# Kernel tuning notes

Measured on AMD Instinct MI355X. Metric: run time of the kernel, lower is better.

## Reference

```python
import jax, jax.numpy as jnp
import numpy as np

WS = 4        # window size
NH = 8        # num heads
GN_GROUPS = 8 # min(8, hidden_dim)
EPS = 1e-5


def group_norm(x, gamma, beta, groups=GN_GROUPS, eps=EPS):
    # x: [B, C, H, W]
    B, C, H, W = x.shape
    xr = x.reshape(B, groups, C // groups, H, W)
    mu = xr.mean(axis=(2, 3, 4), keepdims=True)
    var = xr.var(axis=(2, 3, 4), keepdims=True)
    xn = ((xr - mu) / jnp.sqrt(var + eps)).reshape(B, C, H, W)
    return xn * gamma[None, :, None, None] + beta[None, :, None, None]


def setup_inputs() -> dict:
    key = jax.random.key(0)
    ks = jax.random.split(key, 8)
    B, Cin, Ch, H, W = 4, 64, 256, 128, 128
    sc = 0.02
    return {
        "x": jax.random.normal(ks[0], (B, Cin, H, W), dtype=jnp.float32),
        "h": jax.random.normal(ks[1], (B, Ch, H, W), dtype=jnp.float32),
        "c": jax.random.normal(ks[2], (B, Ch, H, W), dtype=jnp.float32),
        "in_proj_w": jax.random.normal(ks[3], (Ch, Cin + Ch), dtype=jnp.float32) * sc,
        "in_proj_b": jnp.zeros((Ch,), jnp.float32),
        "ln_g": jnp.ones((Ch,), jnp.float32),
        "ln_b": jnp.zeros((Ch,), jnp.float32),
        "qkv_w": jax.random.normal(ks[4], (3 * Ch, Ch), dtype=jnp.float32) * sc,
        "qkv_b": jnp.zeros((3 * Ch,), jnp.float32),
        "proj_w": jax.random.normal(ks[5], (Ch, Ch), dtype=jnp.float32) * sc,
        "proj_b": jnp.zeros((Ch,), jnp.float32),
        "gates_w": jax.random.normal(ks[6], (4 * Ch, Ch), dtype=jnp.float32) * sc,
        "gates_b": jnp.zeros((4 * Ch,), jnp.float32),
        "gn_g": jnp.ones((Ch,), jnp.float32),
        "gn_b": jnp.zeros((Ch,), jnp.float32),
    }


def reference(x, h, c, in_proj_w, in_proj_b, ln_g, ln_b, qkv_w, qkv_b,
              proj_w, proj_b, gates_w, gates_b, gn_g, gn_b):
    B, Cin, H, W = x.shape
    Ch = h.shape[1]
    ws, nh = WS, NH
    hd = Ch // nh
    nHw, nWw = H // ws, W // ws  # H,W divisible by ws -> no padding branch

    # in_proj: 1x1 conv on concat([x, h])
    comb = jnp.concatenate([x, h], axis=1)  # [B, Cin+Ch, H, W]
    p = jnp.einsum('bchw,oc->bohw', comb, in_proj_w) + in_proj_b[None, :, None, None]

    # window partition -> [B*nWin, ws*ws, Ch]
    xw = p.reshape(B, Ch, nHw, ws, nWw, ws)
    xw = xw.transpose(0, 2, 4, 3, 5, 1).reshape(B * nHw * nWw, ws * ws, Ch)

    # pre-attention LayerNorm
    mu = xw.mean(-1, keepdims=True)
    var = xw.var(-1, keepdims=True)
    xn = (xw - mu) / jnp.sqrt(var + EPS) * ln_g + ln_b

    # multi-head attention within each 16-token window
    Bw, N, _ = xn.shape
    qkv = (xn @ qkv_w.T + qkv_b).reshape(Bw, N, 3, nh, hd)
    q, k, v = qkv[:, :, 0], qkv[:, :, 1], qkv[:, :, 2]  # [Bw, N, nh, hd]
    attn = jnp.einsum('bqhd,bkhd->bhqk', q, k) * (hd ** -0.5)
    attn = jax.nn.softmax(attn, axis=-1)
    out = jnp.einsum('bhqk,bkhd->bqhd', attn, v).reshape(Bw, N, Ch)
    out = out @ proj_w.T + proj_b

    # window unpartition -> [B, Ch, H, W]
    am = out.reshape(B, nHw, nWw, ws, ws, Ch)
    am = am.transpose(0, 5, 1, 3, 2, 4).reshape(B, Ch, H, W)

    am = group_norm(am, gn_g, gn_b)  # eval mode: dropout2d is identity

    # LSTM gates via 1x1 conv
    gates = jnp.einsum('bchw,oc->bohw', am, gates_w) + gates_b[None, :, None, None]
    ci, cf, co, cg = jnp.split(gates, 4, axis=1)
    i = jax.nn.sigmoid(ci)
    f = jax.nn.sigmoid(cf)
    o = jax.nn.sigmoid(co)
    g = jnp.tanh(cg)
    cnext = f * c + i * g
    hnext = group_norm(o * jnp.tanh(cnext), gn_g, gn_b)
    return hnext, cnext
```

## Files before the change

kernel.cpp:

```cpp
#include <hip/hip_runtime.h>

#define DI __device__ __forceinline__

typedef unsigned short ushort_t;
typedef __attribute__((ext_vector_type(8))) short bf16x8;
typedef __attribute__((ext_vector_type(4))) float f32x4;
typedef __attribute__((ext_vector_type(4))) unsigned short us4;
typedef __attribute__((ext_vector_type(8))) unsigned short us8;

constexpr float EPSF = 1e-5f;

constexpr size_t O_WIP  = 0;
constexpr size_t O_WQKV = 163840;
constexpr size_t O_WPRJ = 557056;
constexpr size_t O_WGAT = 688128;
constexpr size_t O_GN   = 1736704;
constexpr size_t O_FIN  = 1737216;
constexpr size_t O_R2   = 1740800;
constexpr size_t O_R3   = O_R2 + 33554432;
constexpr size_t O_R1   = O_R3 + 33554432;

DI ushort_t f2b(float f) {
  unsigned u = __float_as_uint(f);
  u += 0x7fff + ((u >> 16) & 1);
  return (ushort_t)(u >> 16);
}
DI float b2f(ushort_t s) { return __uint_as_float(((unsigned)s) << 16); }

DI float fsig(float x) { return 1.f / (1.f + __expf(-x)); }
DI float ftanh(float x) {
  const float e = __expf(-2.f * fabsf(x));
  const float t = (1.f - e) / (1.f + e);
  return copysignf(t, x);
}

DI void cp16(ushort_t* lds, const ushort_t* g) {
  __builtin_amdgcn_global_load_lds(
      (const __attribute__((address_space(1))) unsigned*)g,
      (__attribute__((address_space(3))) unsigned*)lds, 16, 0, 0);
}

__global__ __launch_bounds__(256) void k_prep(const float* __restrict__ ipw,
    const float* __restrict__ qkvw, const float* __restrict__ projw,
    const float* __restrict__ gatesw, ushort_t* __restrict__ d0,
    ushort_t* __restrict__ d1, ushort_t* __restrict__ d2, ushort_t* __restrict__ d3) {
  int i = blockIdx.x * 256 + threadIdx.x;
  if (i < 81920)  { d0[i] = f2b(ipw[i]);    return; }
  i -= 81920;
  if (i < 196608) { d1[i] = f2b(qkvw[i]);   return; }
  i -= 196608;
  if (i < 65536)  { d2[i] = f2b(projw[i]);  return; }
  i -= 65536;
  if (i < 262144) { d3[i] = f2b(gatesw[i]); return; }
}

__global__ __launch_bounds__(256) void k_comb(const float* __restrict__ x,
    const float* __restrict__ h, ushort_t* __restrict__ comb) {
  __shared__ float tile[32][257];
  const int tid = threadIdx.x;
  const int wid = blockIdx.x;
  const int b = wid / 640, r = wid % 640, ct = r / 64, pt = r % 64;
  const int p0 = pt * 256;
#pragma unroll 8
  for (int i = 0; i < 32; ++i) {
    const int cg = ct * 32 + i;
    const float* src = (cg < 64) ? x + (((size_t)(b * 64 + cg)) << 14)
                                 : h + (((size_t)(b * 256 + (cg - 64))) << 14);
    tile[i][tid] = src[p0 + tid];
  }
  __syncthreads();
  const int c = tid & 31;
#pragma unroll 8
  for (int i2 = 0; i2 < 32; ++i2) {
    const int tl = (tid >> 5) + i2 * 8;
    comb[(size_t)((b << 14) + p0 + tl) * 320 + ct * 32 + c] = f2b(tile[c][tl]);
  }
}

template<int K, int KT, bool GATESB>
DI void gemm_main(const ushort_t* __restrict__ A, const ushort_t* __restrict__ B,
                  int t0, int nb, ushort_t* smem, f32x4 acc[4][4]) {
  const int tid = threadIdx.x;
  const int lane = tid & 63, wave = tid >> 6;
  const int w2 = wave * 2;
  const int wm = wave >> 1, wn = wave & 1;
  const int kfs = lane >> 4, cc = lane & 15;
  const int aoff = kfs * 1024 + (wm * 64 + cc) * 8;
  const int boff = 4096 + kfs * 1024 + (wn * 64 + cc) * 8;

  auto stage = [&](int buf, int k0) {
#pragma unroll
    for (int i = 0; i < 2; ++i) {
      const int w2i = w2 + i;
      const int kslot = w2i >> 1;
      const int mrow = ((w2i & 1) << 6) + lane;
      const ushort_t* ga = A + (size_t)(t0 + mrow) * K + k0 + kslot * 8;
      cp16(smem + buf * 8192 + w2i * 512, ga);
      int ng;
      if (GATESB) ng = ((mrow >> 4) & 3) * 256 + nb + ((mrow >> 6) << 4) + (mrow & 15);
      else        ng = nb + mrow;
      const ushort_t* gb = B + (size_t)ng * K + k0 + kslot * 8;
      cp16(smem + buf * 8192 + 4096 + w2i * 512, gb);
    }
  };

  stage(0, 0);
  __syncthreads();
  for (int kt = 0; kt < KT; ++kt) {
    const int cur = (kt & 1) * 8192;
    if (kt + 1 < KT) stage((kt & 1) ^ 1, (kt + 1) * 32);
    bf16x8 a0 = *(const bf16x8*)(smem + cur + aoff);
    bf16x8 a1 = *(const bf16x8*)(smem + cur + aoff + 128);
    bf16x8 a2 = *(const bf16x8*)(smem + cur + aoff + 256);
    bf16x8 a3 = *(const bf16x8*)(smem + cur + aoff + 384);
    bf16x8 b0 = *(const bf16x8*)(smem + cur + boff);
    bf16x8 b1 = *(const bf16x8*)(smem + cur + boff + 128);
    bf16x8 b2 = *(const bf16x8*)(smem + cur + boff + 256);
    bf16x8 b3 = *(const bf16x8*)(smem + cur + boff + 384);
    acc[0][0] = __builtin_amdgcn_mfma_f32_16x16x32_bf16(a0, b0, acc[0][0], 0, 0, 0);
    acc[0][1] = __builtin_amdgcn_mfma_f32_16x16x32_bf16(a0, b1, acc[0][1], 0, 0, 0);
    acc[0][2] = __builtin_amdgcn_mfma_f32_16x16x32_bf16(a0, b2, acc[0][2], 0, 0, 0);
    acc[0][3] = __builtin_amdgcn_mfma_f32_16x16x32_bf16(a0, b3, acc[0][3], 0, 0, 0);
    acc[1][0] = __builtin_amdgcn_mfma_f32_16x16x32_bf16(a1, b0, acc[1][0], 0, 0, 0);
    acc[1][1] = __builtin_amdgcn_mfma_f32_16x16x32_bf16(a1, b1, acc[1][1], 0, 0, 0);
    acc[1][2] = __builtin_amdgcn_mfma_f32_16x16x32_bf16(a1, b2, acc[1][2], 0, 0, 0);
    acc[1][3] = __builtin_amdgcn_mfma_f32_16x16x32_bf16(a1, b3, acc[1][3], 0, 0, 0);
    acc[2][0] = __builtin_amdgcn_mfma_f32_16x16x32_bf16(a2, b0, acc[2][0], 0, 0, 0);
    acc[2][1] = __builtin_amdgcn_mfma_f32_16x16x32_bf16(a2, b1, acc[2][1], 0, 0, 0);
    acc[2][2] = __builtin_amdgcn_mfma_f32_16x16x32_bf16(a2, b2, acc[2][2], 0, 0, 0);
    acc[2][3] = __builtin_amdgcn_mfma_f32_16x16x32_bf16(a2, b3, acc[2][3], 0, 0, 0);
    acc[3][0] = __builtin_amdgcn_mfma_f32_16x16x32_bf16(a3, b0, acc[3][0], 0, 0, 0);
    acc[3][1] = __builtin_amdgcn_mfma_f32_16x16x32_bf16(a3, b1, acc[3][1], 0, 0, 0);
    acc[3][2] = __builtin_amdgcn_mfma_f32_16x16x32_bf16(a3, b2, acc[3][2], 0, 0, 0);
    acc[3][3] = __builtin_amdgcn_mfma_f32_16x16x32_bf16(a3, b3, acc[3][3], 0, 0, 0);
    __syncthreads();
  }
}

template<int NTOT>
DI void epi_store(f32x4 acc[4][4], ushort_t* __restrict__ C, const float* __restrict__ bias,
                  int t0, int n0g) {
  const int tid = threadIdx.x, lane = tid & 63, wave = tid >> 6;
  const int wm = wave >> 1, wn = wave & 1;
  const int r0 = (lane >> 4) * 4, cc = lane & 15;
#pragma unroll
  for (int fn = 0; fn < 4; ++fn) {
    const int n = wn * 64 + fn * 16 + cc;
    const float bv = bias[n0g + n];
#pragma unroll
    for (int fm = 0; fm < 4; ++fm) {
#pragma unroll
      for (int r = 0; r < 4; ++r) {
        const int m = wm * 64 + fm * 16 + r0 + r;
        C[(size_t)(t0 + m) * NTOT + n0g + n] = f2b(acc[fm][fn][r] + bv);
      }
    }
  }
}

__global__ __launch_bounds__(256) void k_inproj_ln(const ushort_t* __restrict__ A,
    const ushort_t* __restrict__ B, const float* __restrict__ bias,
    const float* __restrict__ lg, const float* __restrict__ lb, ushort_t* __restrict__ xn) {
  __shared__ ushort_t smem[20480];
  __shared__ float red[4][2][64];
  __shared__ float fin[2][64];
  const int tid = threadIdx.x, lane = tid & 63, wave = tid >> 6;
  const int t0 = blockIdx.x * 64;
  const int kfs = lane >> 4, cc = lane & 15;
  const int r0 = kfs * 4;
  const int aoff = kfs * 512 + cc * 8;
  const int boff = 2048 + kfs * 2048 + (wave * 64 + cc) * 8;

  auto stage = [&](int buf, int k0) {
#pragma unroll
    for (int rr = 0; rr < 5; ++rr) {
      const int r = wave * 5 + rr;
      const int e = r * 64 + lane;
      const ushort_t* src;
      if (r < 4) src = A + (size_t)(t0 + (e & 63)) * 320 + k0 + (e >> 6) * 8;
      else { const int e2 = e - 256; src = B + (size_t)(e2 & 255) * 320 + k0 + (e2 >> 8) * 8; }
      cp16(smem + buf * 10240 + r * 512, src);
    }
  };

  stage(0, 0);
  f32x4 acc[4][4] = {};
  __syncthreads();
  for (int kt = 0; kt < 10; ++kt) {
    const int cur = (kt & 1) * 10240;
    if (kt < 9) stage((kt & 1) ^ 1, (kt + 1) * 32);
    bf16x8 av[4], bv[4];
#pragma unroll
    for (int i = 0; i < 4; ++i) av[i] = *(const bf16x8*)(smem + cur + aoff + i * 128);
#pragma unroll
    for (int j = 0; j < 4; ++j) bv[j] = *(const bf16x8*)(smem + cur + boff + j * 128);
#pragma unroll
    for (int i = 0; i < 4; ++i)
#pragma unroll
      for (int j = 0; j < 4; ++j)
        acc[i][j] = __builtin_amdgcn_mfma_f32_16x16x32_bf16(av[i], bv[j], acc[i][j], 0, 0, 0);
    __syncthreads();
  }
  float bcol[4];
#pragma unroll
  for (int j = 0; j < 4; ++j) bcol[j] = bias[wave * 64 + j * 16 + cc];
#pragma unroll
  for (int i = 0; i < 4; ++i)
#pragma unroll
    for (int j = 0; j < 4; ++j)
#pragma unroll
      for (int r = 0; r < 4; ++r) acc[i][j][r] += bcol[j];
#pragma unroll
  for (int i = 0; i < 4; ++i) {
#pragma unroll
    for (int r = 0; r < 4; ++r) {
      float s  = acc[i][0][r] + acc[i][1][r] + acc[i][2][r] + acc[i][3][r];
      float s2 = acc[i][0][r] * acc[i][0][r] + acc[i][1][r] * acc[i][1][r]
               + acc[i][2][r] * acc[i][2][r] + acc[i][3][r] * acc[i][3][r];
#pragma unroll
      for (int m = 1; m < 16; m <<= 1) { s += __shfl_xor(s, m); s2 += __shfl_xor(s2, m); }
      if (cc == 0) { red[wave][0][i * 16 + r0 + r] = s; red[wave][1][i * 16 + r0 + r] = s2; }
    }
  }
  __syncthreads();
  if (tid < 64) {
    const float s  = red[0][0][tid] + red[1][0][tid] + red[2][0][tid] + red[3][0][tid];
    const float s2 = red[0][1][tid] + red[1][1][tid] + red[2][1][tid] + red[3][1][tid];
    const float m = s * (1.f / 256.f);
    const float var = s2 * (1.f / 256.f) - m * m;
    fin[0][tid] = m;
    fin[1][tid] = rsqrtf(fmaxf(var, 0.f) + EPSF);
  }
  __syncthreads();
  float lgv[4], lbv[4];
#pragma unroll
  for (int j = 0; j < 4; ++j) {
    const int n = wave * 64 + j * 16 + cc;
    lgv[j] = lg[n]; lbv[j] = lb[n];
  }
#pragma unroll
  for (int i = 0; i < 4; ++i)
#pragma unroll
    for (int r = 0; r < 4; ++r) {
      const int m = i * 16 + r0 + r;
      const float mu = fin[0][m], rs = fin[1][m];
      ushort_t* dst = xn + (size_t)(t0 + m) * 256 + wave * 64 + cc;
#pragma unroll
      for (int j = 0; j < 4; ++j)
        dst[j * 16] = f2b((acc[i][j][r] - mu) * rs * lgv[j] + lbv[j]);
    }
}

__global__ __launch_bounds__(256) void k_qkv(const ushort_t* __restrict__ A,
    const ushort_t* __restrict__ B, const float* __restrict__ bias, ushort_t* __restrict__ C) {
  __shared__ ushort_t smem[16384];
  const int wid = blockIdx.x, g = wid & 7, s = wid >> 3;
  const int mt = g * 64 + s / 6, nt = s % 6;
  f32x4 acc[4][4] = {};
  gemm_main<256, 8, false>(A, B, mt * 128, nt * 128, smem, acc);
  epi_store<768>(acc, C, bias, mt * 128, nt * 128);
}

__global__ __launch_bounds__(256) void k_proj(const ushort_t* __restrict__ A,
    const ushort_t* __restrict__ B, const float* __restrict__ bias, ushort_t* __restrict__ C,
    float* __restrict__ gnsum) {
  __shared__ ushort_t smem[16384];
  const int wid = blockIdx.x, g = wid & 7, s = wid >> 3;
  const int mt = g * 64 + s / 2, nt = s % 2;
  const int t0 = mt * 128, n0g = nt * 128;
  f32x4 acc[4][4] = {};
  gemm_main<256, 8, false>(A, B, t0, n0g, smem, acc);
  const int tid = threadIdx.x, lane = tid & 63, wave = tid >> 6;
  const int wm = wave >> 1, wn = wave & 1;
  const int r0 = (lane >> 4) * 4, cc = lane & 15;
  float sA = 0.f, s2A = 0.f, sB = 0.f, s2B = 0.f;
#pragma unroll
  for (int fn = 0; fn < 4; ++fn) {
    const int n = wn * 64 + fn * 16 + cc;
    const float bv = bias[n0g + n];
#pragma unroll
    for (int fm = 0; fm < 4; ++fm) {
#pragma unroll
      for (int r = 0; r < 4; ++r) {
        const int m = wm * 64 + fm * 16 + r0 + r;
        const float v = acc[fm][fn][r] + bv;
        C[(size_t)(t0 + m) * 256 + n0g + n] = f2b(v);
        if (fn < 2) { sA += v; s2A += v * v; } else { sB += v; s2B += v * v; }
      }
    }
  }
#pragma unroll
  for (int o = 32; o; o >>= 1) {
    sA += __shfl_down(sA, o); s2A += __shfl_down(s2A, o);
    sB += __shfl_down(sB, o); s2B += __shfl_down(s2B, o);
  }
  if (lane == 0) {
    const int bch = t0 >> 14;
    const int gb0 = (n0g >> 5) + wn * 2;
    atomicAdd(&gnsum[bch * 8 + gb0], sA);      atomicAdd(&gnsum[32 + bch * 8 + gb0], s2A);
    atomicAdd(&gnsum[bch * 8 + gb0 + 1], sB);  atomicAdd(&gnsum[32 + bch * 8 + gb0 + 1], s2B);
  }
}

__global__ __launch_bounds__(256) void k_gates(const ushort_t* __restrict__ A,
    const ushort_t* __restrict__ B, const float* __restrict__ gbias,
    const float* __restrict__ cin, float* __restrict__ cnext, float* __restrict__ u,
    float* __restrict__ gnsum2) {
  __shared__ ushort_t smem[16384];
  const int wid = blockIdx.x, g = wid & 7, s = wid >> 3;
  const int mt = g * 64 + (s >> 3), nt = s & 7;
  const int t0 = mt * 128, ch0 = nt * 32;
  f32x4 acc[4][4] = {};
  gemm_main<256, 8, true>(A, B, t0, ch0, smem, acc);

  const int tid = threadIdx.x, lane = tid & 63, wave = tid >> 6;
  const int wm = wave >> 1, wn = wave & 1;
  const int r0 = (lane >> 4) * 4, cc = lane & 15;
  const int bch = t0 >> 14, pix0 = t0 & 16383;
  const int ch = ch0 + wn * 16 + cc;
  const float bi = gbias[ch], bf_ = gbias[256 + ch];
  const float bo = gbias[512 + ch], bg = gbias[768 + ch];
  const size_t chbase = ((size_t)(bch * 256 + ch)) << 14;
  float ssum = 0.f, ssq = 0.f;
#pragma unroll
  for (int fm = 0; fm < 4; ++fm) {
    const int pix = pix0 + wm * 64 + fm * 16 + r0;
    const float4 cv = *(const float4*)(cin + chbase + pix);
    float cn[4], uv[4];
#pragma unroll
    for (int r = 0; r < 4; ++r) {
      const float iv = fsig(acc[fm][0][r] + bi);
      const float fv = fsig(acc[fm][1][r] + bf_);
      const float ov = fsig(acc[fm][2][r] + bo);
      const float gv = ftanh(acc[fm][3][r] + bg);
      const float cold = (&cv.x)[r];
      const float c2 = fv * cold + iv * gv;
      cn[r] = c2;
      const float uu = ov * ftanh(c2);
      uv[r] = uu; ssum += uu; ssq += uu * uu;
    }
    *(float4*)(cnext + chbase + pix) = *(float4*)cn;
    *(float4*)(u + chbase + pix)     = *(float4*)uv;
  }
#pragma unroll
  for (int o = 32; o; o >>= 1) { ssum += __shfl_down(ssum, o); ssq += __shfl_down(ssq, o); }
  if (lane == 0) {
    atomicAdd(&gnsum2[bch * 8 + nt], ssum);
    atomicAdd(&gnsum2[32 + bch * 8 + nt], ssq);
  }
}

__global__ __launch_bounds__(128) void k_attn(const ushort_t* __restrict__ qkvb,
    ushort_t* __restrict__ ao) {
  __shared__ float ks[4224], vs[4224];
  const int tid = threadIdx.x;
  const int wid = blockIdx.x;
  const int b = wid >> 10, rem = wid & 1023, wh = rem >> 5, wc = rem & 31;
  const int tbase = (b << 14) + wh * 512 + wc * 4;
#pragma unroll 4
  for (int it = 0; it < 16; ++it) {
    const int i = it * 128 + tid;
    const int j = i >> 7, q = i & 127;
    const int which = q >> 6, hh2 = (q >> 3) & 7, d4 = (q & 7) << 2;
    const int tj = tbase + ((j >> 2) << 7) + (j & 3);
    us4 v = *(const us4*)(qkvb + (size_t)tj * 768 + 256 + which * 256 + hh2 * 32 + d4);
    float* dst = (which ? vs : ks) + (hh2 * 16 + j) * 33 + d4;
    dst[0] = b2f(v[0]); dst[1] = b2f(v[1]); dst[2] = b2f(v[2]); dst[3] = b2f(v[3]);
  }
  const int hh = tid >> 4, qi = tid & 15;
  const int tq = tbase + ((qi >> 2) << 7) + (qi & 3);
  float qv[32];
  {
    const ushort_t* qp = qkvb + (size_t)tq * 768 + hh * 32;
#pragma unroll
    for (int uq = 0; uq < 8; ++uq) {
      us4 v = *(const us4*)(qp + uq * 4);
#pragma unroll
      for (int e = 0; e < 4; ++e) qv[uq * 4 + e] = b2f(v[e]);
    }
  }
  __syncthreads();
  float sc[16];
#pragma unroll
  for (int j = 0; j < 16; ++j) {
    const float* kr = ks + (hh * 16 + j) * 33;
    float s = 0.f;
#pragma unroll
    for (int u2 = 0; u2 < 32; ++u2) s = fmaf(qv[u2], kr[u2], s);
    sc[j] = s * 0.17677669529663687f;
  }
  float m = sc[0];
#pragma unroll
  for (int j = 1; j < 16; ++j) m = fmaxf(m, sc[j]);
  float ssum = 0.f;
#pragma unroll
  for (int j = 0; j < 16; ++j) { sc[j] = __expf(sc[j] - m); ssum += sc[j]; }
  const float inv = 1.f / ssum;
  float oacc[32] = {};
#pragma unroll
  for (int j = 0; j < 16; ++j) {
    const float p = sc[j] * inv;
    const float* vr = vs + (hh * 16 + j) * 33;
#pragma unroll
    for (int u2 = 0; u2 < 32; ++u2) oacc[u2] = fmaf(p, vr[u2], oacc[u2]);
  }
  unsigned* dst = (unsigned*)(ao + (size_t)tq * 256 + hh * 32);
#pragma unroll
  for (int uq = 0; uq < 16; ++uq)
    dst[uq] = (unsigned)f2b(oacc[2 * uq]) | ((unsigned)f2b(oacc[2 * uq + 1]) << 16);
}

__global__ void k_gnfin(const float* __restrict__ sums, float* __restrict__ fin) {
  const int i = threadIdx.x;
  const float invN = 1.f / 524288.f;
  const float m = sums[i] * invN;
  const float var = sums[32 + i] * invN - m * m;
  fin[i] = m;
  fin[32 + i] = rsqrtf(fmaxf(var, 0.f) + EPSF);
}

__global__ __launch_bounds__(256) void k_amn(const ushort_t* __restrict__ am,
    const float* __restrict__ fin, const float* __restrict__ gg,
    const float* __restrict__ gb, ushort_t* __restrict__ amn) {
  const size_t i = ((size_t)blockIdx.x * 256 + threadIdx.x) * 8;
  const int t = (int)(i >> 8), c = (int)(i & 255);
  const int b = t >> 14, grp = c >> 5;
  const float m = fin[b * 8 + grp], r = fin[32 + b * 8 + grp];
  us8 v = *(const us8*)(am + i);
  us8 o;
#pragma unroll
  for (int e = 0; e < 8; ++e)
    o[e] = f2b((b2f(v[e]) - m) * r * gg[c + e] + gb[c + e]);
  *(us8*)(amn + i) = o;
}

__global__ __launch_bounds__(256) void k_gnapply(const float* __restrict__ u,
    const float* __restrict__ fin2, const float* __restrict__ gg,
    const float* __restrict__ gb, float* __restrict__ hout) {
  const size_t base = ((size_t)blockIdx.x * 256 + threadIdx.x) * 4;
  const int b = (int)(base >> 22);
  const int ch = (int)((base >> 14) & 255);
  const int grp = ch >> 5;
  const float m = fin2[b * 8 + grp], r = fin2[32 + b * 8 + grp];
  const float gv = gg[ch], bv = gb[ch];
  float4 v = *(const float4*)(u + base);
  v.x = (v.x - m) * r * gv + bv;
  v.y = (v.y - m) * r * gv + bv;
  v.z = (v.z - m) * r * gv + bv;
  v.w = (v.w - m) * r * gv + bv;
  *(float4*)(hout + base) = v;
}

extern "C" void kernel_launch(void* const* d_in, const int* in_sizes, int n_in,
                              void* d_out, int out_size, void* d_ws, size_t ws_size,
                              hipStream_t stream) {
  const float* x      = (const float*)d_in[0];
  const float* h      = (const float*)d_in[1];
  const float* c      = (const float*)d_in[2];
  const float* ipw    = (const float*)d_in[3];
  const float* ipb    = (const float*)d_in[4];
  const float* lng    = (const float*)d_in[5];
  const float* lnb    = (const float*)d_in[6];
  const float* qkvw   = (const float*)d_in[7];
  const float* qkvb   = (const float*)d_in[8];
  const float* projw  = (const float*)d_in[9];
  const float* projb  = (const float*)d_in[10];
  const float* gatesw = (const float*)d_in[11];
  const float* gatesb = (const float*)d_in[12];
  const float* gng    = (const float*)d_in[13];
  const float* gnb    = (const float*)d_in[14];
  char* wsb  = (char*)d_ws;
  float* out = (float*)d_out;

  ushort_t* wip  = (ushort_t*)(wsb + O_WIP);
  ushort_t* wqkv = (ushort_t*)(wsb + O_WQKV);
  ushort_t* wprj = (ushort_t*)(wsb + O_WPRJ);
  ushort_t* wgat = (ushort_t*)(wsb + O_WGAT);
  float* gnsum   = (float*)(wsb + O_GN);
  float* gnfin   = (float*)(wsb + O_FIN);
  ushort_t* R2   = (ushort_t*)(wsb + O_R2);
  ushort_t* R3   = (ushort_t*)(wsb + O_R3);
  ushort_t* R1   = (ushort_t*)(wsb + O_R1);

  hipMemsetAsync(gnsum, 0, 512, stream);
  k_prep<<<2368, 256, 0, stream>>>(ipw, qkvw, projw, gatesw, wip, wqkv, wprj, wgat);
  k_comb<<<2560, 256, 0, stream>>>(x, h, R1);
  k_inproj_ln<<<1024, 256, 0, stream>>>(R1, wip, ipb, lng, lnb, R3);
  k_qkv<<<3072, 256, 0, stream>>>(R3, wqkv, qkvb, R1);
  k_attn<<<4096, 128, 0, stream>>>(R1, R2);
  k_proj<<<1024, 256, 0, stream>>>(R2, wprj, projb, R3, gnsum);
  k_gnfin<<<1, 32, 0, stream>>>(gnsum, gnfin);
  k_amn<<<8192, 256, 0, stream>>>(R3, gnfin, gng, gnb, R2);
  k_gates<<<4096, 256, 0, stream>>>(R2, wgat, gatesb, c, out + 16777216, (float*)R1,
                                    gnsum + 64);
  k_gnfin<<<1, 32, 0, stream>>>(gnsum + 64, gnfin + 64);
  k_gnapply<<<16384, 256, 0, stream>>>((float*)R1, gnfin + 64, gng, gnb, out);
}
```

Before: 789.5 us.

## Triple-buffer GEMM LDS staging with vmcnt waits; vectorize attention LDS layout

The shared GEMM mainloop and the in_proj+LN kernel move from double to triple buffering. Loads are issued two k-tiles ahead, and the full __syncthreads is replaced by an explicit s_waitcnt vmcnt plus barrier, which lets more global-to-LDS traffic overlap with MFMA work. The attention kernel's K/V shared layout changes from a padded stride-33 scalar layout to a 32-float row layout with a per-head stride of 516, so the dot products and accumulation can use float4 LDS reads. The cost is more LDS per block (lower occupancy) and possible bank conflicts from the unpadded rows.

```diff
diff --git a/kernel.cpp b/kernel.cpp
--- a/kernel.cpp
+++ b/kernel.cpp
@@ -39,6 +39,14 @@
       (const __attribute__((address_space(1))) unsigned*)g,
       (__attribute__((address_space(3))) unsigned*)lds, 16, 0, 0);
 }
+
+template<int N> DI void vm_wait() {
+  if constexpr (N == 0)      asm volatile("s_waitcnt vmcnt(0)" ::: "memory");
+  else if constexpr (N == 4) asm volatile("s_waitcnt vmcnt(4)" ::: "memory");
+  else if constexpr (N == 5) asm volatile("s_waitcnt vmcnt(5)" ::: "memory");
+}
+DI void sbar() { __builtin_amdgcn_s_barrier(); }
+DI void sb0()  { __builtin_amdgcn_sched_barrier(0); }
 
 __global__ __launch_bounds__(256) void k_prep(const float* __restrict__ ipw,
     const float* __restrict__ qkvw, const float* __restrict__ projw,
@@ -105,10 +113,12 @@
   };
 
   stage(0, 0);
-  __syncthreads();
+  stage(1, 32);
+  vm_wait<4>(); sbar(); sb0();
+#pragma unroll
   for (int kt = 0; kt < KT; ++kt) {
-    const int cur = (kt & 1) * 8192;
-    if (kt + 1 < KT) stage((kt & 1) ^ 1, (kt + 1) * 32);
+    const int cur = (kt % 3) * 8192;
+    if (kt + 2 < KT) stage((kt + 2) % 3, (kt + 2) * 32);
     bf16x8 a0 = *(const bf16x8*)(smem + cur + aoff);
     bf16x8 a1 = *(const bf16x8*)(smem + cur + aoff + 128);
     bf16x8 a2 = *(const bf16x8*)(smem + cur + aoff + 256);
@@ -133,7 +143,10 @@
     acc[3][1] = __builtin_amdgcn_mfma_f32_16x16x32_bf16(a3, b1, acc[3][1], 0, 0, 0);
     acc[3][2] = __builtin_amdgcn_mfma_f32_16x16x32_bf16(a3, b2, acc[3][2], 0, 0, 0);
     acc[3][3] = __builtin_amdgcn_mfma_f32_16x16x32_bf16(a3, b3, acc[3][3], 0, 0, 0);
-    __syncthreads();
+    if (kt + 1 < KT) {
+      if (kt + 2 < KT) vm_wait<4>(); else vm_wait<0>();
+      sbar(); sb0();
+    }
   }
 }
 
@@ -161,7 +174,7 @@
 __global__ __launch_bounds__(256) void k_inproj_ln(const ushort_t* __restrict__ A,
     const ushort_t* __restrict__ B, const float* __restrict__ bias,
     const float* __restrict__ lg, const float* __restrict__ lb, ushort_t* __restrict__ xn) {
-  __shared__ ushort_t smem[20480];
+  __shared__ ushort_t smem[30720];
   __shared__ float red[4][2][64];
   __shared__ float fin[2][64];
   const int tid = threadIdx.x, lane = tid & 63, wave = tid >> 6;
@@ -184,11 +197,13 @@
   };
 
   stage(0, 0);
+  stage(1, 32);
   f32x4 acc[4][4] = {};
-  __syncthreads();
+  vm_wait<5>(); sbar(); sb0();
+#pragma unroll
   for (int kt = 0; kt < 10; ++kt) {
-    const int cur = (kt & 1) * 10240;
-    if (kt < 9) stage((kt & 1) ^ 1, (kt + 1) * 32);
+    const int cur = (kt % 3) * 10240;
+    if (kt + 2 < 10) stage((kt + 2) % 3, (kt + 2) * 32);
     bf16x8 av[4], bv[4];
 #pragma unroll
     for (int i = 0; i < 4; ++i) av[i] = *(const bf16x8*)(smem + cur + aoff + i * 128);
@@ -199,7 +214,10 @@
 #pragma unroll
       for (int j = 0; j < 4; ++j)
         acc[i][j] = __builtin_amdgcn_mfma_f32_16x16x32_bf16(av[i], bv[j], acc[i][j], 0, 0, 0);
-    __syncthreads();
+    if (kt + 1 < 10) {
+      if (kt + 2 < 10) vm_wait<5>(); else vm_wait<0>();
+      sbar(); sb0();
+    }
   }
   float bcol[4];
 #pragma unroll
@@ -253,7 +271,7 @@
 
 __global__ __launch_bounds__(256) void k_qkv(const ushort_t* __restrict__ A,
     const ushort_t* __restrict__ B, const float* __restrict__ bias, ushort_t* __restrict__ C) {
-  __shared__ ushort_t smem[16384];
+  __shared__ ushort_t smem[24576];
   const int wid = blockIdx.x, g = wid & 7, s = wid >> 3;
   const int mt = g * 64 + s / 6, nt = s % 6;
   f32x4 acc[4][4] = {};
@@ -264,7 +282,7 @@
 __global__ __launch_bounds__(256) void k_proj(const ushort_t* __restrict__ A,
     const ushort_t* __restrict__ B, const float* __restrict__ bias, ushort_t* __restrict__ C,
     float* __restrict__ gnsum) {
-  __shared__ ushort_t smem[16384];
+  __shared__ ushort_t smem[24576];
   const int wid = blockIdx.x, g = wid & 7, s = wid >> 3;
   const int mt = g * 64 + s / 2, nt = s % 2;
   const int t0 = mt * 128, n0g = nt * 128;
@@ -306,7 +324,7 @@
     const ushort_t* __restrict__ B, const float* __restrict__ gbias,
     const float* __restrict__ cin, float* __restrict__ cnext, float* __restrict__ u,
     float* __restrict__ gnsum2) {
-  __shared__ ushort_t smem[16384];
+  __shared__ ushort_t smem[24576];
   const int wid = blockIdx.x, g = wid & 7, s = wid >> 3;
   const int mt = g * 64 + (s >> 3), nt = s & 7;
   const int t0 = mt * 128, ch0 = nt * 32;
@@ -352,20 +370,22 @@
 
 __global__ __launch_bounds__(128) void k_attn(const ushort_t* __restrict__ qkvb,
     ushort_t* __restrict__ ao) {
-  __shared__ float ks[4224], vs[4224];
+  __shared__ float ks[4128], vs[4128];
   const int tid = threadIdx.x;
   const int wid = blockIdx.x;
   const int b = wid >> 10, rem = wid & 1023, wh = rem >> 5, wc = rem & 31;
   const int tbase = (b << 14) + wh * 512 + wc * 4;
-#pragma unroll 4
-  for (int it = 0; it < 16; ++it) {
-    const int i = it * 128 + tid;
-    const int j = i >> 7, q = i & 127;
-    const int which = q >> 6, hh2 = (q >> 3) & 7, d4 = (q & 7) << 2;
-    const int tj = tbase + ((j >> 2) << 7) + (j & 3);
-    us4 v = *(const us4*)(qkvb + (size_t)tj * 768 + 256 + which * 256 + hh2 * 32 + d4);
-    float* dst = (which ? vs : ks) + (hh2 * 16 + j) * 33 + d4;
-    dst[0] = b2f(v[0]); dst[1] = b2f(v[1]); dst[2] = b2f(v[2]); dst[3] = b2f(v[3]);
+  {
+    const int which = tid >> 6, hh2 = (tid >> 3) & 7, d4 = (tid & 7) << 2;
+    float* base = (which ? vs : ks) + hh2 * 516 + d4;
+    const ushort_t* gsrc = qkvb + 256 + which * 256 + hh2 * 32 + d4;
+#pragma unroll
+    for (int j = 0; j < 16; ++j) {
+      const int tj = tbase + ((j >> 2) << 7) + (j & 3);
+      us4 v = *(const us4*)(gsrc + (size_t)tj * 768);
+      float* dst = base + j * 32;
+      dst[0] = b2f(v[0]); dst[1] = b2f(v[1]); dst[2] = b2f(v[2]); dst[3] = b2f(v[3]);
+    }
   }
   const int hh = tid >> 4, qi = tid & 15;
   const int tq = tbase + ((qi >> 2) << 7) + (qi & 3);
@@ -383,10 +403,16 @@
   float sc[16];
 #pragma unroll
   for (int j = 0; j < 16; ++j) {
-    const float* kr = ks + (hh * 16 + j) * 33;
+    const float4* kr = (const float4*)(ks + hh * 516 + j * 32);
     float s = 0.f;
 #pragma unroll
-    for (int u2 = 0; u2 < 32; ++u2) s = fmaf(qv[u2], kr[u2], s);
+    for (int u2 = 0; u2 < 8; ++u2) {
+      const float4 kk = kr[u2];
+      s = fmaf(qv[u2 * 4], kk.x, s);
+      s = fmaf(qv[u2 * 4 + 1], kk.y, s);
+      s = fmaf(qv[u2 * 4 + 2], kk.z, s);
+      s = fmaf(qv[u2 * 4 + 3], kk.w, s);
+    }
     sc[j] = s * 0.17677669529663687f;
   }
   float m = sc[0];
@@ -396,18 +422,26 @@
 #pragma unroll
   for (int j = 0; j < 16; ++j) { sc[j] = __expf(sc[j] - m); ssum += sc[j]; }
   const float inv = 1.f / ssum;
-  float oacc[32] = {};
+  float4 oacc[8] = {};
 #pragma unroll
   for (int j = 0; j < 16; ++j) {
     const float p = sc[j] * inv;
-    const float* vr = vs + (hh * 16 + j) * 33;
-#pragma unroll
-    for (int u2 = 0; u2 < 32; ++u2) oacc[u2] = fmaf(p, vr[u2], oacc[u2]);
+    const float4* vr = (const float4*)(vs + hh * 516 + j * 32);
+#pragma unroll
+    for (int u2 = 0; u2 < 8; ++u2) {
+      const float4 vv = vr[u2];
+      oacc[u2].x = fmaf(p, vv.x, oacc[u2].x);
+      oacc[u2].y = fmaf(p, vv.y, oacc[u2].y);
+      oacc[u2].z = fmaf(p, vv.z, oacc[u2].z);
+      oacc[u2].w = fmaf(p, vv.w, oacc[u2].w);
+    }
   }
   unsigned* dst = (unsigned*)(ao + (size_t)tq * 256 + hh * 32);
 #pragma unroll
-  for (int uq = 0; uq < 16; ++uq)
-    dst[uq] = (unsigned)f2b(oacc[2 * uq]) | ((unsigned)f2b(oacc[2 * uq + 1]) << 16);
+  for (int u2 = 0; u2 < 8; ++u2) {
+    dst[u2 * 2]     = (unsigned)f2b(oacc[u2].x) | ((unsigned)f2b(oacc[u2].y) << 16);
+    dst[u2 * 2 + 1] = (unsigned)f2b(oacc[u2].z) | ((unsigned)f2b(oacc[u2].w) << 16);
+  }
 }
 
 __global__ void k_gnfin(const float* __restrict__ sums, float* __restrict__ fin) {
```

Result: faster. 749.0 us (-5.1%).
